# Performance work log

Hardware: AMD Instinct MI355X
Metric: run time of the kernel (lower is better)

The kernel has to match this reference:

```python
import jax, jax.numpy as jnp
import numpy as np

HID = 64        # hid_size
NUM_LAYER = 3
NG = 16         # number of graphs in batch
NPG = 160       # nodes per graph
N = NG * NPG    # 2560 total nodes
DEG = 16
EPG = NPG * DEG # edges per graph
E = NG * EPG    # 40960 total edges
P = NG * NPG * NPG  # 409600 total (i,j) pairs from triu_indices(n, -n)
AV = 64         # atom feature vocab per column (9 columns)
BV = 8          # bond feature vocab per column (3 columns)
EPS = 1e-5


def setup_inputs() -> dict:
    rng = np.random.default_rng(0)
    key = jax.random.key(0)
    ks = jax.random.split(key, 16)

    # categorical node / edge features
    x = jnp.asarray(rng.integers(0, AV, size=(N, 9)), dtype=jnp.int32)
    edge_attr = jnp.asarray(rng.integers(0, BV, size=(E, 3)), dtype=jnp.int32)

    # within-graph random edges (sorted order not required for the math here)
    src_l = rng.integers(0, NPG, size=(NG, EPG))
    dst_l = rng.integers(0, NPG, size=(NG, EPG))
    gid = np.repeat(np.arange(NG), EPG)
    # flat position of edge (u,v) of graph g inside the concatenated all-pairs list
    epos = jnp.asarray(gid * NPG * NPG + src_l.reshape(-1) * NPG + dst_l.reshape(-1),
                       dtype=jnp.int32)

    # idx = concat([triu_indices(n, -n) + ptr[g]]) -> all pairs, row-major per graph
    g = np.arange(NG)[:, None, None]
    i = np.arange(NPG)[None, :, None]
    j = np.arange(NPG)[None, None, :]
    idx0 = jnp.asarray(np.broadcast_to(g * NPG + i, (NG, NPG, NPG)).reshape(-1).astype(np.int32))
    idx1 = jnp.asarray(np.broadcast_to(g * NPG + j, (NG, NPG, NPG)).reshape(-1).astype(np.int32))

    def lin(k, fan_in, fan_out):
        b = 1.0 / np.sqrt(fan_in)
        kw, kb = jax.random.split(k)
        return (jax.random.uniform(kw, (fan_in, fan_out), jnp.float32, -b, b),
                jax.random.uniform(kb, (fan_out,), jnp.float32, -b, b))

    atom_tables = jax.random.normal(ks[0], (9, AV, HID), jnp.float32) * 0.02
    bond_tables = jax.random.normal(ks[1], (3, BV, HID), jnp.float32) * 0.02
    W1, b1 = lin(ks[2], HID, HID)
    W2, b2 = lin(ks[3], HID, HID)
    We, be = lin(ks[4], HID, HID)
    L0_w, L0_b = lin(ks[5], 3 * HID, HID)
    L1_w, L1_b = lin(ks[6], HID, HID)
    L2_w, L2_b = lin(ks[7], HID, 1)
    g0 = jnp.ones((HID,), jnp.float32); beta0 = jnp.zeros((HID,), jnp.float32)
    g1 = jnp.ones((HID,), jnp.float32); beta1 = jnp.zeros((HID,), jnp.float32)

    return dict(atom_tables=atom_tables, bond_tables=bond_tables,
                W1=W1, b1=b1, W2=W2, b2=b2, We=We, be=be,
                L0_w=L0_w, L0_b=L0_b, L1_w=L1_w, L1_b=L1_b, L2_w=L2_w, L2_b=L2_b,
                g0=g0, beta0=beta0, g1=g1, beta1=beta1,
                x=x, edge_attr=edge_attr, idx0=idx0, idx1=idx1, epos=epos)


def _batchnorm(h, gamma, beta):
    mu = jnp.mean(h, axis=0)
    var = jnp.mean(jnp.square(h - mu), axis=0)  # biased var, torch training mode
    return (h - mu) * jax.lax.rsqrt(var + EPS) * gamma + beta


def reference(atom_tables, bond_tables, W1, b1, W2, b2, We, be,
              L0_w, L0_b, L1_w, L1_b, L2_w, L2_b,
              g0, beta0, g1, beta1,
              x, edge_attr, idx0, idx1, epos):
    # AtomEncoder / BondEncoder: sum of per-column embedding lookups
    cols9 = jnp.arange(9)[None, :]
    x_emb = atom_tables[cols9, x].sum(axis=1)          # [N, HID]
    cols3 = jnp.arange(3)[None, :]
    ea_emb = bond_tables[cols3, edge_attr].sum(axis=1)  # [E, HID]

    n1 = (x_emb @ W1 + b1)[idx0]                        # [P, HID]
    n2 = (x_emb @ W2 + b2)[idx1]                        # [P, HID]

    e = ea_emb @ We + be                                # [E, HID]
    # equivalent of SparseTensor.to_dense()[idx0, idx1] without the N^2 dense blowup;
    # duplicate edges sum, missing pairs are zero (matches to_dense semantics)
    e_pairs = jnp.zeros((P, HID), e.dtype).at[epos].add(e)

    emb = jnp.concatenate((n1, n2, e_pairs), axis=-1)   # [P, 3*HID]

    emb = jax.nn.relu(_batchnorm(emb @ L0_w + L0_b, g0, beta0))
    emb = jax.nn.relu(_batchnorm(emb @ L1_w + L1_b, g1, beta1))
    emb = emb @ L2_w + L2_b                             # [P, 1]
    return jnp.squeeze(emb, axis=-1)                    # [P]
```

## Files before the change

### kernel.cpp

```cpp
#include <hip/hip_runtime.h>
#include <hip/hip_bf16.h>

#define HID 64
#define NGr 16
#define NPG 160
#define NN  2560
#define EE  40960
#define PPG 25600
#define PT  409600
#define AV  64
#define BV  8
#define EPSB 1e-5f

typedef __attribute__((ext_vector_type(8))) short short8v;
typedef __attribute__((ext_vector_type(4))) float f32x4;

static __device__ __forceinline__ unsigned short bf16_hi(float v) {
    return (unsigned short)(__float_as_uint(v) >> 16);
}
static __device__ __forceinline__ float bf16_val(unsigned short h) {
    return __uint_as_float(((unsigned int)h) << 16);
}

__global__ void k_prep(const float* __restrict__ W1, const float* __restrict__ b1,
                       const float* __restrict__ W2, const float* __restrict__ b2,
                       const float* __restrict__ We, const float* __restrict__ be,
                       const float* __restrict__ L0w, const float* __restrict__ L0b,
                       const float* __restrict__ L1w,
                       float* __restrict__ W1c, float* __restrict__ W2c, float* __restrict__ Wec,
                       float* __restrict__ b1c, float* __restrict__ b2c, float* __restrict__ bec,
                       float* __restrict__ stats,
                       unsigned short* __restrict__ WBhi, unsigned short* __restrict__ WBlo) {
    int blk = blockIdx.x, tid = threadIdx.x;
    if (blk == 3) {
        stats[tid] = 0.f;
        for (int idx = tid; idx < 4096; idx += 256) {
            float w = L1w[idx];
            unsigned short hi = bf16_hi(w);
            float rem = w - bf16_val(hi);
            WBhi[idx] = hi;
            WBlo[idx] = bf16_hi(rem);
        }
        return;
    }
    const float* Wsrc = (blk == 0) ? W1 : (blk == 1) ? W2 : We;
    const float* bsrc = (blk == 0) ? b1 : (blk == 1) ? b2 : be;
    const float* L    = L0w + blk * 64 * 64;
    float* Wdst = (blk == 0) ? W1c : (blk == 1) ? W2c : Wec;
    float* bdst = (blk == 0) ? b1c : (blk == 1) ? b2c : bec;
    for (int idx = tid; idx < 4096; idx += 256) {
        int k = idx >> 6, h = idx & 63;
        float acc = 0.f;
        for (int m = 0; m < 64; ++m) acc = fmaf(Wsrc[k * 64 + m], L[m * 64 + h], acc);
        Wdst[idx] = acc;
    }
    if (tid < 64) {
        int h = tid;
        float acc = (blk == 0) ? L0b[h] : 0.f;
        for (int m = 0; m < 64; ++m) acc = fmaf(bsrc[m], L[m * 64 + h], acc);
        bdst[h] = acc;
    }
}

__global__ void k_nodes(const float* __restrict__ atab, const int* __restrict__ x,
                        const float* __restrict__ W1c, const float* __restrict__ W2c,
                        const float* __restrict__ b1c, const float* __restrict__ b2c,
                        float* __restrict__ A, float* __restrict__ Bm) {
    int n = blockIdx.x, h = threadIdx.x;
    __shared__ float xe[64];
    float v = 0.f;
#pragma unroll
    for (int c = 0; c < 9; ++c) v += atab[c * AV * HID + x[n * 9 + c] * HID + h];
    xe[h] = v;
    __syncthreads();
    float a = b1c[h], b = b2c[h];
#pragma unroll
    for (int k = 0; k < 64; ++k) {
        float xk = xe[k];
        a = fmaf(xk, W1c[k * 64 + h], a);
        b = fmaf(xk, W2c[k * 64 + h], b);
    }
    A[n * 64 + h] = a;
    Bm[n * 64 + h] = b;
}

__global__ void __launch_bounds__(256) k_dense(const float* __restrict__ A, const float* __restrict__ Bm,
                                               float* __restrict__ zbuf, float* __restrict__ stats) {
    int h = threadIdx.x & 63;
    int wid = threadIdx.x >> 6;
    int wavesTotal = gridDim.x * 4;
    int wave = blockIdx.x * 4 + wid;
    float s = 0.f, ss = 0.f;
    for (int row = wave; row < PT; row += wavesTotal) {
        int g = row / PPG;
        int rem = row - g * PPG;
        int i = rem / NPG;
        int j = rem - i * NPG;
        float v = A[(g * NPG + i) * 64 + h] + Bm[(g * NPG + j) * 64 + h];
        zbuf[(size_t)row * 64 + h] = v;
        s += v;
        ss = fmaf(v, v, ss);
    }
    __shared__ float ls[128];
    if (threadIdx.x < 128) ls[threadIdx.x] = 0.f;
    __syncthreads();
    atomicAdd(&ls[h], s);
    atomicAdd(&ls[64 + h], ss);
    __syncthreads();
    if (threadIdx.x < 128) atomicAdd(&stats[threadIdx.x], ls[threadIdx.x]);
}

__global__ void __launch_bounds__(256) k_edges(const float* __restrict__ btab, const int* __restrict__ eattr,
                                               const int* __restrict__ epos,
                                               const float* __restrict__ Wec, const float* __restrict__ bec,
                                               float* __restrict__ zbuf, float* __restrict__ stats) {
    int h = threadIdx.x & 63;
    int el = threadIdx.x >> 6;
    __shared__ float ea[4][64];
    float s = 0.f, ss = 0.f;
    for (int base = blockIdx.x * 4; base < EE; base += gridDim.x * 4) {
        int e = base + el;
        float v = 0.f;
#pragma unroll
        for (int c = 0; c < 3; ++c) v += btab[c * BV * HID + eattr[e * 3 + c] * HID + h];
        ea[el][h] = v;
        __syncthreads();
        float ew = bec[h];
#pragma unroll
        for (int k = 0; k < 64; ++k) ew = fmaf(ea[el][k], Wec[k * 64 + h], ew);
        int p = epos[e];
        float old = atomicAdd(&zbuf[(size_t)p * 64 + h], ew);
        s += ew;
        ss += 2.f * old * ew + ew * ew;
        __syncthreads();
    }
    __shared__ float ls[128];
    if (threadIdx.x < 128) ls[threadIdx.x] = 0.f;
    __syncthreads();
    atomicAdd(&ls[h], s);
    atomicAdd(&ls[64 + h], ss);
    __syncthreads();
    if (threadIdx.x < 128) atomicAdd(&stats[threadIdx.x], ls[threadIdx.x]);
}

__global__ void __launch_bounds__(256) k_mid(const unsigned short* __restrict__ WBhi,
                                             const unsigned short* __restrict__ WBlo,
                                             const float* __restrict__ L1b,
                                             const float* __restrict__ g0, const float* __restrict__ beta0,
                                             float* __restrict__ zbuf, float* __restrict__ stats) {
    int lane = threadIdx.x & 63;
    int wid  = blockIdx.x * 4 + (threadIdx.x >> 6);
    int nWaves = gridDim.x * 4;
    int r16 = lane & 15;
    int kg  = lane >> 4;

    const float invP = 1.f / (float)PT;
    float s0a[8], t0a[8], s0b[8], t0b[8];
#pragma unroll
    for (int j = 0; j < 8; ++j) {
        int k = kg * 8 + j;
        float mu = stats[k] * invP;
        float var = stats[64 + k] * invP - mu * mu;
        float inv = rsqrtf(var + EPSB);
        s0a[j] = g0[k] * inv;
        t0a[j] = fmaf(-mu, s0a[j], beta0[k]);
        int k2 = k + 32;
        float mu2 = stats[k2] * invP;
        float var2 = stats[64 + k2] * invP - mu2 * mu2;
        float inv2 = rsqrtf(var2 + EPSB);
        s0b[j] = g0[k2] * inv2;
        t0b[j] = fmaf(-mu2, s0b[j], beta0[k2]);
    }
    short8v Bhi[4][2], Blo[4][2];
#pragma unroll
    for (int ct = 0; ct < 4; ++ct)
#pragma unroll
        for (int ks = 0; ks < 2; ++ks)
#pragma unroll
            for (int j = 0; j < 8; ++j) {
                int k = ks * 32 + kg * 8 + j;
                int idx = k * 64 + ct * 16 + r16;
                Bhi[ct][ks][j] = (short)WBhi[idx];
                Blo[ct][ks][j] = (short)WBlo[idx];
            }
    float biasv[4];
#pragma unroll
    for (int ct = 0; ct < 4; ++ct) biasv[ct] = L1b[ct * 16 + r16];

    float sum[4] = {0.f, 0.f, 0.f, 0.f}, ssum[4] = {0.f, 0.f, 0.f, 0.f};

    for (int tile = wid; tile < PT / 16; tile += nWaves) {
        float* tb = zbuf + (size_t)tile * 16 * 64;
        const float4 za0 = *reinterpret_cast<const float4*>(tb + r16 * 64 + kg * 8);
        const float4 za1 = *reinterpret_cast<const float4*>(tb + r16 * 64 + kg * 8 + 4);
        const float4 zb0 = *reinterpret_cast<const float4*>(tb + r16 * 64 + 32 + kg * 8);
        const float4 zb1 = *reinterpret_cast<const float4*>(tb + r16 * 64 + 32 + kg * 8 + 4);
        float ha[8] = {za0.x, za0.y, za0.z, za0.w, za1.x, za1.y, za1.z, za1.w};
        float hb[8] = {zb0.x, zb0.y, zb0.z, zb0.w, zb1.x, zb1.y, zb1.z, zb1.w};
        short8v aHi0, aLo0, aHi1, aLo1;
#pragma unroll
        for (int j = 0; j < 8; ++j) {
            float hv = fmaxf(fmaf(ha[j], s0a[j], t0a[j]), 0.f);
            unsigned short hi = bf16_hi(hv);
            float rem = hv - bf16_val(hi);
            aHi0[j] = (short)hi;
            aLo0[j] = (short)bf16_hi(rem);
            float hv2 = fmaxf(fmaf(hb[j], s0b[j], t0b[j]), 0.f);
            unsigned short hi2 = bf16_hi(hv2);
            float rem2 = hv2 - bf16_val(hi2);
            aHi1[j] = (short)hi2;
            aLo1[j] = (short)bf16_hi(rem2);
        }
        f32x4 acc[4];
#pragma unroll
        for (int ct = 0; ct < 4; ++ct) acc[ct] = (f32x4){0.f, 0.f, 0.f, 0.f};
#pragma unroll
        for (int ct = 0; ct < 4; ++ct) {
            acc[ct] = __builtin_amdgcn_mfma_f32_16x16x32_bf16(aHi0, Bhi[ct][0], acc[ct], 0, 0, 0);
            acc[ct] = __builtin_amdgcn_mfma_f32_16x16x32_bf16(aHi0, Blo[ct][0], acc[ct], 0, 0, 0);
            acc[ct] = __builtin_amdgcn_mfma_f32_16x16x32_bf16(aLo0, Bhi[ct][0], acc[ct], 0, 0, 0);
            acc[ct] = __builtin_amdgcn_mfma_f32_16x16x32_bf16(aHi1, Bhi[ct][1], acc[ct], 0, 0, 0);
            acc[ct] = __builtin_amdgcn_mfma_f32_16x16x32_bf16(aHi1, Blo[ct][1], acc[ct], 0, 0, 0);
            acc[ct] = __builtin_amdgcn_mfma_f32_16x16x32_bf16(aLo1, Bhi[ct][1], acc[ct], 0, 0, 0);
        }
#pragma unroll
        for (int ct = 0; ct < 4; ++ct) {
#pragma unroll
            for (int reg = 0; reg < 4; ++reg) {
                float z = acc[ct][reg] + biasv[ct];
                tb[(kg * 4 + reg) * 64 + ct * 16 + r16] = z;
                sum[ct] += z;
                ssum[ct] = fmaf(z, z, ssum[ct]);
            }
        }
    }
#pragma unroll
    for (int ct = 0; ct < 4; ++ct) {
        float s = sum[ct];
        s += __shfl_xor(s, 16);
        s += __shfl_xor(s, 32);
        float q = ssum[ct];
        q += __shfl_xor(q, 16);
        q += __shfl_xor(q, 32);
        if (kg == 0) {
            atomicAdd(&stats[128 + ct * 16 + r16], s);
            atomicAdd(&stats[192 + ct * 16 + r16], q);
        }
    }
}

__global__ void __launch_bounds__(256) k_final(const float* __restrict__ g1, const float* __restrict__ beta1,
                                               const float* __restrict__ L2w, const float* __restrict__ L2b,
                                               const float* __restrict__ zbuf, float* __restrict__ out,
                                               const float* __restrict__ stats) {
    int lane = threadIdx.x & 63;
    int wid = threadIdx.x >> 6;
    int q = lane & 15;
    int rl = lane >> 4;
    const float invP = 1.f / (float)PT;
    float s1[4], t1[4], wv[4];
#pragma unroll
    for (int c = 0; c < 4; ++c) {
        int col = q * 4 + c;
        float mu = stats[128 + col] * invP;
        float var = stats[192 + col] * invP - mu * mu;
        float inv = rsqrtf(var + EPSB);
        s1[c] = g1[col] * inv;
        t1[c] = fmaf(-mu, s1[c], beta1[col]);
        wv[c] = L2w[col];
    }
    float bias = L2b[0];
    int waveId = blockIdx.x * 4 + wid;
    int stride = gridDim.x * 16;
    for (int base = waveId * 4; base < PT; base += stride) {
        const float4 zv = *reinterpret_cast<const float4*>(zbuf + (size_t)base * 64 + lane * 4);
        float p;
        p  = fmaxf(fmaf(zv.x, s1[0], t1[0]), 0.f) * wv[0];
        p  = fmaf(fmaxf(fmaf(zv.y, s1[1], t1[1]), 0.f), wv[1], p);
        p  = fmaf(fmaxf(fmaf(zv.z, s1[2], t1[2]), 0.f), wv[2], p);
        p  = fmaf(fmaxf(fmaf(zv.w, s1[3], t1[3]), 0.f), wv[3], p);
        p += __shfl_xor(p, 1);
        p += __shfl_xor(p, 2);
        p += __shfl_xor(p, 4);
        p += __shfl_xor(p, 8);
        if (q == 0) out[base + rl] = p + bias;
    }
}

extern "C" void kernel_launch(void* const* d_in, const int* in_sizes, int n_in,
                              void* d_out, int out_size, void* d_ws, size_t ws_size,
                              hipStream_t stream) {
    const float* atab  = (const float*)d_in[0];
    const float* btab  = (const float*)d_in[1];
    const float* W1    = (const float*)d_in[2];
    const float* b1    = (const float*)d_in[3];
    const float* W2    = (const float*)d_in[4];
    const float* b2    = (const float*)d_in[5];
    const float* We    = (const float*)d_in[6];
    const float* be    = (const float*)d_in[7];
    const float* L0w   = (const float*)d_in[8];
    const float* L0b   = (const float*)d_in[9];
    const float* L1w   = (const float*)d_in[10];
    const float* L1b   = (const float*)d_in[11];
    const float* L2w   = (const float*)d_in[12];
    const float* L2b   = (const float*)d_in[13];
    const float* g0    = (const float*)d_in[14];
    const float* beta0 = (const float*)d_in[15];
    const float* g1    = (const float*)d_in[16];
    const float* beta1 = (const float*)d_in[17];
    const int*   x     = (const int*)d_in[18];
    const int*   eattr = (const int*)d_in[19];
    const int*   epos  = (const int*)d_in[22];
    float* out = (float*)d_out;

    float* ws = (float*)d_ws;
    float* zbuf = ws;
    float* A    = zbuf + (size_t)PT * 64;
    float* Bm   = A + NN * 64;
    float* W1c  = Bm + NN * 64;
    float* W2c  = W1c + 4096;
    float* Wec  = W2c + 4096;
    float* b1c  = Wec + 4096;
    float* b2c  = b1c + 64;
    float* bec  = b2c + 64;
    float* stats = bec + 64;
    unsigned short* WBhi = (unsigned short*)(stats + 256);
    unsigned short* WBlo = WBhi + 4096;

    k_prep<<<4, 256, 0, stream>>>(W1, b1, W2, b2, We, be, L0w, L0b, L1w,
                                  W1c, W2c, Wec, b1c, b2c, bec, stats, WBhi, WBlo);
    k_nodes<<<NN, 64, 0, stream>>>(atab, x, W1c, W2c, b1c, b2c, A, Bm);
    k_dense<<<2048, 256, 0, stream>>>(A, Bm, zbuf, stats);
    k_edges<<<512, 256, 0, stream>>>(btab, eattr, epos, Wec, bec, zbuf, stats);
    k_mid<<<512, 256, 0, stream>>>(WBhi, WBlo, L1b, g0, beta0, zbuf, stats);
    k_final<<<1024, 256, 0, stream>>>(g1, beta1, L2w, L2b, zbuf, out, stats);
}
```

Before: 231.4 us.

## Eliminate dense pair buffer; recompute layer-0/1 per tile from node and edge lists

```diff
diff --git a/kernel.cpp b/kernel.cpp
--- a/kernel.cpp
+++ b/kernel.cpp
@@ -8,6 +8,8 @@
 #define EE  40960
 #define PPG 25600
 #define PT  409600
+#define TT  25600
+#define TPG 1600
 #define AV  64
 #define BV  8
 #define EPSB 1e-5f
@@ -29,11 +31,9 @@
                        const float* __restrict__ L1w,
                        float* __restrict__ W1c, float* __restrict__ W2c, float* __restrict__ Wec,
                        float* __restrict__ b1c, float* __restrict__ b2c, float* __restrict__ bec,
-                       float* __restrict__ stats,
                        unsigned short* __restrict__ WBhi, unsigned short* __restrict__ WBlo) {
     int blk = blockIdx.x, tid = threadIdx.x;
     if (blk == 3) {
-        stats[tid] = 0.f;
         for (int idx = tid; idx < 4096; idx += 256) {
             float w = L1w[idx];
             unsigned short hi = bf16_hi(w);
@@ -84,78 +84,195 @@
     Bm[n * 64 + h] = b;
 }
 
-__global__ void __launch_bounds__(256) k_dense(const float* __restrict__ A, const float* __restrict__ Bm,
-                                               float* __restrict__ zbuf, float* __restrict__ stats) {
-    int h = threadIdx.x & 63;
-    int wid = threadIdx.x >> 6;
-    int wavesTotal = gridDim.x * 4;
-    int wave = blockIdx.x * 4 + wid;
-    float s = 0.f, ss = 0.f;
-    for (int row = wave; row < PT; row += wavesTotal) {
-        int g = row / PPG;
-        int rem = row - g * PPG;
-        int i = rem / NPG;
-        int j = rem - i * NPG;
-        float v = A[(g * NPG + i) * 64 + h] + Bm[(g * NPG + j) * 64 + h];
-        zbuf[(size_t)row * 64 + h] = v;
-        s += v;
-        ss = fmaf(v, v, ss);
-    }
-    __shared__ float ls[128];
-    if (threadIdx.x < 128) ls[threadIdx.x] = 0.f;
+__global__ void k_gstats(const float* __restrict__ A, const float* __restrict__ Bm,
+                         float* __restrict__ stats) {
+    int g = blockIdx.x;
+    int h = threadIdx.x & 63, w = threadIdx.x >> 6;
+    float sA = 0.f, sA2 = 0.f, sB = 0.f, sB2 = 0.f;
+    for (int n = w; n < NPG; n += 4) {
+        float a = A[(size_t)(g * NPG + n) * 64 + h];
+        float b = Bm[(size_t)(g * NPG + n) * 64 + h];
+        sA += a; sA2 = fmaf(a, a, sA2);
+        sB += b; sB2 = fmaf(b, b, sB2);
+    }
+    __shared__ float ls[4][4][64];
+    ls[w][0][h] = sA; ls[w][1][h] = sA2; ls[w][2][h] = sB; ls[w][3][h] = sB2;
     __syncthreads();
-    atomicAdd(&ls[h], s);
-    atomicAdd(&ls[64 + h], ss);
-    __syncthreads();
-    if (threadIdx.x < 128) atomicAdd(&stats[threadIdx.x], ls[threadIdx.x]);
+    if (w == 0) {
+        sA  = ls[0][0][h] + ls[1][0][h] + ls[2][0][h] + ls[3][0][h];
+        sA2 = ls[0][1][h] + ls[1][1][h] + ls[2][1][h] + ls[3][1][h];
+        sB  = ls[0][2][h] + ls[1][2][h] + ls[2][2][h] + ls[3][2][h];
+        sB2 = ls[0][3][h] + ls[1][3][h] + ls[2][3][h] + ls[3][3][h];
+        atomicAdd(&stats[h], 160.f * (sA + sB));
+        atomicAdd(&stats[64 + h], 160.f * (sA2 + sB2) + 2.f * sA * sB);
+    }
 }
 
 __global__ void __launch_bounds__(256) k_edges(const float* __restrict__ btab, const int* __restrict__ eattr,
                                                const int* __restrict__ epos,
                                                const float* __restrict__ Wec, const float* __restrict__ bec,
-                                               float* __restrict__ zbuf, float* __restrict__ stats) {
+                                               float* __restrict__ ewf, float* __restrict__ stats,
+                                               int* __restrict__ bcount) {
     int h = threadIdx.x & 63;
     int el = threadIdx.x >> 6;
     __shared__ float ea[4][64];
-    float s = 0.f, ss = 0.f;
+    float ssum = 0.f;
     for (int base = blockIdx.x * 4; base < EE; base += gridDim.x * 4) {
         int e = base + el;
         float v = 0.f;
 #pragma unroll
         for (int c = 0; c < 3; ++c) v += btab[c * BV * HID + eattr[e * 3 + c] * HID + h];
         ea[el][h] = v;
+        float ew = bec[h];
+#pragma unroll
+        for (int k = 0; k < 64; ++k) ew = fmaf(ea[el][k], Wec[k * 64 + h], ew);
+        ewf[(size_t)e * 64 + h] = ew;
+        ssum += ew;
+        if (h == 0) atomicAdd(&bcount[epos[e] >> 4], 1);
+    }
+    atomicAdd(&stats[h], ssum);
+}
+
+__global__ void k_scan(const int* __restrict__ bcount, int* __restrict__ boffs,
+                       int* __restrict__ bcursor) {
+    __shared__ int part[256];
+    int tid = threadIdx.x;
+    int base = tid * (TT / 256);
+    int s = 0;
+    for (int q = 0; q < TT / 256; ++q) s += bcount[base + q];
+    part[tid] = s;
+    __syncthreads();
+    for (int d = 1; d < 256; d <<= 1) {
+        int v = (tid >= d) ? part[tid - d] : 0;
         __syncthreads();
-        float ew = bec[h];
-#pragma unroll
-        for (int k = 0; k < 64; ++k) ew = fmaf(ea[el][k], Wec[k * 64 + h], ew);
-        int p = epos[e];
-        float old = atomicAdd(&zbuf[(size_t)p * 64 + h], ew);
-        s += ew;
-        ss += 2.f * old * ew + ew * ew;
+        part[tid] += v;
         __syncthreads();
     }
-    __shared__ float ls[128];
-    if (threadIdx.x < 128) ls[threadIdx.x] = 0.f;
-    __syncthreads();
-    atomicAdd(&ls[h], s);
-    atomicAdd(&ls[64 + h], ss);
-    __syncthreads();
-    if (threadIdx.x < 128) atomicAdd(&stats[threadIdx.x], ls[threadIdx.x]);
-}
-
-__global__ void __launch_bounds__(256) k_mid(const unsigned short* __restrict__ WBhi,
-                                             const unsigned short* __restrict__ WBlo,
-                                             const float* __restrict__ L1b,
-                                             const float* __restrict__ g0, const float* __restrict__ beta0,
-                                             float* __restrict__ zbuf, float* __restrict__ stats) {
-    int lane = threadIdx.x & 63;
-    int wid  = blockIdx.x * 4 + (threadIdx.x >> 6);
-    int nWaves = gridDim.x * 4;
-    int r16 = lane & 15;
-    int kg  = lane >> 4;
-
+    int run = part[tid] - s;
+    for (int q = 0; q < TT / 256; ++q) {
+        int c = bcount[base + q];
+        boffs[base + q] = run;
+        bcursor[base + q] = run;
+        run += c;
+    }
+    if (tid == 255) boffs[TT] = run;
+}
+
+__global__ void k_fill(const int* __restrict__ epos, int* __restrict__ bcursor,
+                       int* __restrict__ elist) {
+    int e = blockIdx.x * 256 + threadIdx.x;
+    if (e >= EE) return;
+    int p = epos[e];
+    int t = p >> 4, jj = p & 15;
+    int slot = atomicAdd(&bcursor[t], 1);
+    elist[slot] = (e << 4) | jj;
+}
+
+__global__ void __launch_bounds__(256) k_scorr(const float* __restrict__ A, const float* __restrict__ Bm,
+                                               const float* __restrict__ ewf,
+                                               const int* __restrict__ boffs, const int* __restrict__ elist,
+                                               float* __restrict__ stats) {
+    __shared__ float run[4][16][64];
+    int h = threadIdx.x & 63, w = threadIdx.x >> 6;
+#pragma unroll
+    for (int jj = 0; jj < 16; ++jj) run[w][jj][h] = 0.f;
+    float ssacc = 0.f;
+    int wave = blockIdx.x * 4 + w;
+    int nw = gridDim.x * 4;
+    for (int t = wave; t < TT; t += nw) {
+        int be = boffs[t], en = boffs[t + 1];
+        if (be == en) continue;
+        int g = t / TPG;
+        int rem = t - g * TPG;
+        int i = rem / 10;
+        int j0 = (rem - i * 10) << 4;
+        float a = A[(size_t)(g * NPG + i) * 64 + h];
+        for (int q = be; q < en; ++q) {
+            int pk = elist[q];
+            int e = pk >> 4, jj = pk & 15;
+            float ew = ewf[(size_t)e * 64 + h];
+            float base = a + Bm[(size_t)(g * NPG + j0 + jj) * 64 + h];
+            float r = run[w][jj][h];
+            ssacc += 2.f * (base + r) * ew + ew * ew;
+            run[w][jj][h] = r + ew;
+        }
+        for (int q = be; q < en; ++q) run[w][elist[q] & 15][h] = 0.f;
+    }
+    atomicAdd(&stats[64 + h], ssacc);
+}
+
+static __device__ __forceinline__ void compute_tile(
+    int tile, int r16, int kg,
+    const float* __restrict__ A, const float* __restrict__ Bm, const float* __restrict__ ewf,
+    const int* __restrict__ boffs, const int* __restrict__ elist,
+    const float* s0a, const float* t0a, const float* s0b, const float* t0b,
+    const short8v Bhi[4][2], const short8v Blo[4][2],
+    f32x4 acc[4]) {
+    int g = tile / TPG;
+    int rem = tile - g * TPG;
+    int i = rem / 10;
+    int j0 = (rem - i * 10) << 4;
+    const float* Arow = A + (size_t)(g * NPG + i) * 64;
+    const float* Brow = Bm + (size_t)(g * NPG + j0 + r16) * 64;
+    float4 a0 = *reinterpret_cast<const float4*>(Arow + kg * 8);
+    float4 a1 = *reinterpret_cast<const float4*>(Arow + kg * 8 + 4);
+    float4 a2 = *reinterpret_cast<const float4*>(Arow + 32 + kg * 8);
+    float4 a3 = *reinterpret_cast<const float4*>(Arow + 32 + kg * 8 + 4);
+    float4 b0 = *reinterpret_cast<const float4*>(Brow + kg * 8);
+    float4 b1 = *reinterpret_cast<const float4*>(Brow + kg * 8 + 4);
+    float4 b2 = *reinterpret_cast<const float4*>(Brow + 32 + kg * 8);
+    float4 b3 = *reinterpret_cast<const float4*>(Brow + 32 + kg * 8 + 4);
+    float za[8] = {a0.x + b0.x, a0.y + b0.y, a0.z + b0.z, a0.w + b0.w,
+                   a1.x + b1.x, a1.y + b1.y, a1.z + b1.z, a1.w + b1.w};
+    float zb[8] = {a2.x + b2.x, a2.y + b2.y, a2.z + b2.z, a2.w + b2.w,
+                   a3.x + b3.x, a3.y + b3.y, a3.z + b3.z, a3.w + b3.w};
+    int be = boffs[tile], en = boffs[tile + 1];
+    for (int q = be; q < en; ++q) {
+        int pk = elist[q];
+        int e = pk >> 4, jj = pk & 15;
+        const float* er = ewf + (size_t)e * 64;
+        float4 e0 = *reinterpret_cast<const float4*>(er + kg * 8);
+        float4 e1 = *reinterpret_cast<const float4*>(er + kg * 8 + 4);
+        float4 e2 = *reinterpret_cast<const float4*>(er + 32 + kg * 8);
+        float4 e3 = *reinterpret_cast<const float4*>(er + 32 + kg * 8 + 4);
+        if (r16 == jj) {
+            za[0] += e0.x; za[1] += e0.y; za[2] += e0.z; za[3] += e0.w;
+            za[4] += e1.x; za[5] += e1.y; za[6] += e1.z; za[7] += e1.w;
+            zb[0] += e2.x; zb[1] += e2.y; zb[2] += e2.z; zb[3] += e2.w;
+            zb[4] += e3.x; zb[5] += e3.y; zb[6] += e3.z; zb[7] += e3.w;
+        }
+    }
+    short8v aHi0, aLo0, aHi1, aLo1;
+#pragma unroll
+    for (int j = 0; j < 8; ++j) {
+        float hv = fmaxf(fmaf(za[j], s0a[j], t0a[j]), 0.f);
+        unsigned short hi = bf16_hi(hv);
+        float remv = hv - bf16_val(hi);
+        aHi0[j] = (short)hi;
+        aLo0[j] = (short)bf16_hi(remv);
+        float hv2 = fmaxf(fmaf(zb[j], s0b[j], t0b[j]), 0.f);
+        unsigned short hi2 = bf16_hi(hv2);
+        float rem2 = hv2 - bf16_val(hi2);
+        aHi1[j] = (short)hi2;
+        aLo1[j] = (short)bf16_hi(rem2);
+    }
+#pragma unroll
+    for (int ct = 0; ct < 4; ++ct) acc[ct] = (f32x4){0.f, 0.f, 0.f, 0.f};
+#pragma unroll
+    for (int ct = 0; ct < 4; ++ct) {
+        acc[ct] = __builtin_amdgcn_mfma_f32_16x16x32_bf16(aHi0, Bhi[ct][0], acc[ct], 0, 0, 0);
+        acc[ct] = __builtin_amdgcn_mfma_f32_16x16x32_bf16(aHi0, Blo[ct][0], acc[ct], 0, 0, 0);
+        acc[ct] = __builtin_amdgcn_mfma_f32_16x16x32_bf16(aLo0, Bhi[ct][0], acc[ct], 0, 0, 0);
+        acc[ct] = __builtin_amdgcn_mfma_f32_16x16x32_bf16(aHi1, Bhi[ct][1], acc[ct], 0, 0, 0);
+        acc[ct] = __builtin_amdgcn_mfma_f32_16x16x32_bf16(aHi1, Blo[ct][1], acc[ct], 0, 0, 0);
+        acc[ct] = __builtin_amdgcn_mfma_f32_16x16x32_bf16(aLo1, Bhi[ct][1], acc[ct], 0, 0, 0);
+    }
+}
+
+static __device__ __forceinline__ void load_bn0(const float* __restrict__ stats,
+                                                const float* __restrict__ g0, const float* __restrict__ beta0,
+                                                int kg, float* s0a, float* t0a, float* s0b, float* t0b) {
     const float invP = 1.f / (float)PT;
-    float s0a[8], t0a[8], s0b[8], t0b[8];
 #pragma unroll
     for (int j = 0; j < 8; ++j) {
         int k = kg * 8 + j;
@@ -171,7 +288,11 @@
         s0b[j] = g0[k2] * inv2;
         t0b[j] = fmaf(-mu2, s0b[j], beta0[k2]);
     }
-    short8v Bhi[4][2], Blo[4][2];
+}
+
+static __device__ __forceinline__ void load_wb(const unsigned short* __restrict__ WBhi,
+                                               const unsigned short* __restrict__ WBlo,
+                                               int r16, int kg, short8v Bhi[4][2], short8v Blo[4][2]) {
 #pragma unroll
     for (int ct = 0; ct < 4; ++ct)
 #pragma unroll
@@ -183,52 +304,36 @@
                 Bhi[ct][ks][j] = (short)WBhi[idx];
                 Blo[ct][ks][j] = (short)WBlo[idx];
             }
+}
+
+__global__ void __launch_bounds__(256) k_pass1(const unsigned short* __restrict__ WBhi,
+                                               const unsigned short* __restrict__ WBlo,
+                                               const float* __restrict__ L1b,
+                                               const float* __restrict__ g0, const float* __restrict__ beta0,
+                                               const float* __restrict__ A, const float* __restrict__ Bm,
+                                               const float* __restrict__ ewf,
+                                               const int* __restrict__ boffs, const int* __restrict__ elist,
+                                               float* __restrict__ stats) {
+    int lane = threadIdx.x & 63;
+    int wid = blockIdx.x * 4 + (threadIdx.x >> 6);
+    int nWaves = gridDim.x * 4;
+    int r16 = lane & 15, kg = lane >> 4;
+    float s0a[8], t0a[8], s0b[8], t0b[8];
+    load_bn0(stats, g0, beta0, kg, s0a, t0a, s0b, t0b);
+    short8v Bhi[4][2], Blo[4][2];
+    load_wb(WBhi, WBlo, r16, kg, Bhi, Blo);
     float biasv[4];
 #pragma unroll
     for (int ct = 0; ct < 4; ++ct) biasv[ct] = L1b[ct * 16 + r16];
-
     float sum[4] = {0.f, 0.f, 0.f, 0.f}, ssum[4] = {0.f, 0.f, 0.f, 0.f};
-
-    for (int tile = wid; tile < PT / 16; tile += nWaves) {
-        float* tb = zbuf + (size_t)tile * 16 * 64;
-        const float4 za0 = *reinterpret_cast<const float4*>(tb + r16 * 64 + kg * 8);
-        const float4 za1 = *reinterpret_cast<const float4*>(tb + r16 * 64 + kg * 8 + 4);
-        const float4 zb0 = *reinterpret_cast<const float4*>(tb + r16 * 64 + 32 + kg * 8);
-        const float4 zb1 = *reinterpret_cast<const float4*>(tb + r16 * 64 + 32 + kg * 8 + 4);
-        float ha[8] = {za0.x, za0.y, za0.z, za0.w, za1.x, za1.y, za1.z, za1.w};
-        float hb[8] = {zb0.x, zb0.y, zb0.z, zb0.w, zb1.x, zb1.y, zb1.z, zb1.w};
-        short8v aHi0, aLo0, aHi1, aLo1;
-#pragma unroll
-        for (int j = 0; j < 8; ++j) {
-            float hv = fmaxf(fmaf(ha[j], s0a[j], t0a[j]), 0.f);
-            unsigned short hi = bf16_hi(hv);
-            float rem = hv - bf16_val(hi);
-            aHi0[j] = (short)hi;
-            aLo0[j] = (short)bf16_hi(rem);
-            float hv2 = fmaxf(fmaf(hb[j], s0b[j], t0b[j]), 0.f);
-            unsigned short hi2 = bf16_hi(hv2);
-            float rem2 = hv2 - bf16_val(hi2);
-            aHi1[j] = (short)hi2;
-            aLo1[j] = (short)bf16_hi(rem2);
-        }
+    for (int tile = wid; tile < TT; tile += nWaves) {
         f32x4 acc[4];
-#pragma unroll
-        for (int ct = 0; ct < 4; ++ct) acc[ct] = (f32x4){0.f, 0.f, 0.f, 0.f};
-#pragma unroll
-        for (int ct = 0; ct < 4; ++ct) {
-            acc[ct] = __builtin_amdgcn_mfma_f32_16x16x32_bf16(aHi0, Bhi[ct][0], acc[ct], 0, 0, 0);
-            acc[ct] = __builtin_amdgcn_mfma_f32_16x16x32_bf16(aHi0, Blo[ct][0], acc[ct], 0, 0, 0);
-            acc[ct] = __builtin_amdgcn_mfma_f32_16x16x32_bf16(aLo0, Bhi[ct][0], acc[ct], 0, 0, 0);
-            acc[ct] = __builtin_amdgcn_mfma_f32_16x16x32_bf16(aHi1, Bhi[ct][1], acc[ct], 0, 0, 0);
-            acc[ct] = __builtin_amdgcn_mfma_f32_16x16x32_bf16(aHi1, Blo[ct][1], acc[ct], 0, 0, 0);
-            acc[ct] = __builtin_amdgcn_mfma_f32_16x16x32_bf16(aLo1, Bhi[ct][1], acc[ct], 0, 0, 0);
-        }
+        compute_tile(tile, r16, kg, A, Bm, ewf, boffs, elist, s0a, t0a, s0b, t0b, Bhi, Blo, acc);
 #pragma unroll
         for (int ct = 0; ct < 4; ++ct) {
 #pragma unroll
             for (int reg = 0; reg < 4; ++reg) {
                 float z = acc[ct][reg] + biasv[ct];
-                tb[(kg * 4 + reg) * 64 + ct * 16 + r16] = z;
                 sum[ct] += z;
                 ssum[ct] = fmaf(z, z, ssum[ct]);
             }
@@ -249,41 +354,55 @@
     }
 }
 
-__global__ void __launch_bounds__(256) k_final(const float* __restrict__ g1, const float* __restrict__ beta1,
+__global__ void __launch_bounds__(256) k_pass2(const unsigned short* __restrict__ WBhi,
+                                               const unsigned short* __restrict__ WBlo,
+                                               const float* __restrict__ L1b,
+                                               const float* __restrict__ g0, const float* __restrict__ beta0,
+                                               const float* __restrict__ g1, const float* __restrict__ beta1,
                                                const float* __restrict__ L2w, const float* __restrict__ L2b,
-                                               const float* __restrict__ zbuf, float* __restrict__ out,
-                                               const float* __restrict__ stats) {
+                                               const float* __restrict__ A, const float* __restrict__ Bm,
+                                               const float* __restrict__ ewf,
+                                               const int* __restrict__ boffs, const int* __restrict__ elist,
+                                               const float* __restrict__ stats, float* __restrict__ out) {
     int lane = threadIdx.x & 63;
-    int wid = threadIdx.x >> 6;
-    int q = lane & 15;
-    int rl = lane >> 4;
+    int wid = blockIdx.x * 4 + (threadIdx.x >> 6);
+    int nWaves = gridDim.x * 4;
+    int r16 = lane & 15, kg = lane >> 4;
+    float s0a[8], t0a[8], s0b[8], t0b[8];
+    load_bn0(stats, g0, beta0, kg, s0a, t0a, s0b, t0b);
+    short8v Bhi[4][2], Blo[4][2];
+    load_wb(WBhi, WBlo, r16, kg, Bhi, Blo);
+    float biasv[4], s1c[4], t1c[4], wv[4];
     const float invP = 1.f / (float)PT;
-    float s1[4], t1[4], wv[4];
-#pragma unroll
-    for (int c = 0; c < 4; ++c) {
-        int col = q * 4 + c;
+#pragma unroll
+    for (int ct = 0; ct < 4; ++ct) {
+        int col = ct * 16 + r16;
+        biasv[ct] = L1b[col];
         float mu = stats[128 + col] * invP;
         float var = stats[192 + col] * invP - mu * mu;
         float inv = rsqrtf(var + EPSB);
-        s1[c] = g1[col] * inv;
-        t1[c] = fmaf(-mu, s1[c], beta1[col]);
-        wv[c] = L2w[col];
-    }
-    float bias = L2b[0];
-    int waveId = blockIdx.x * 4 + wid;
-    int stride = gridDim.x * 16;
-    for (int base = waveId * 4; base < PT; base += stride) {
-        const float4 zv = *reinterpret_cast<const float4*>(zbuf + (size_t)base * 64 + lane * 4);
-        float p;
-        p  = fmaxf(fmaf(zv.x, s1[0], t1[0]), 0.f) * wv[0];
-        p  = fmaf(fmaxf(fmaf(zv.y, s1[1], t1[1]), 0.f), wv[1], p);
-        p  = fmaf(fmaxf(fmaf(zv.z, s1[2], t1[2]), 0.f), wv[2], p);
-        p  = fmaf(fmaxf(fmaf(zv.w, s1[3], t1[3]), 0.f), wv[3], p);
-        p += __shfl_xor(p, 1);
-        p += __shfl_xor(p, 2);
-        p += __shfl_xor(p, 4);
-        p += __shfl_xor(p, 8);
-        if (q == 0) out[base + rl] = p + bias;
+        s1c[ct] = g1[col] * inv;
+        t1c[ct] = fmaf(-mu, s1c[ct], beta1[col]);
+        wv[ct] = L2w[col];
+    }
+    float obias = L2b[0];
+    for (int tile = wid; tile < TT; tile += nWaves) {
+        f32x4 acc[4];
+        compute_tile(tile, r16, kg, A, Bm, ewf, boffs, elist, s0a, t0a, s0b, t0b, Bhi, Blo, acc);
+#pragma unroll
+        for (int reg = 0; reg < 4; ++reg) {
+            float p = 0.f;
+#pragma unroll
+            for (int ct = 0; ct < 4; ++ct) {
+                float z = acc[ct][reg] + biasv[ct];
+                p = fmaf(fmaxf(fmaf(z, s1c[ct], t1c[ct]), 0.f), wv[ct], p);
+            }
+            p += __shfl_xor(p, 1);
+            p += __shfl_xor(p, 2);
+            p += __shfl_xor(p, 4);
+            p += __shfl_xor(p, 8);
+            if (r16 == 0) out[tile * 16 + kg * 4 + reg] = p + obias;
+        }
     }
 }
 
@@ -313,11 +432,11 @@
     const int*   epos  = (const int*)d_in[22];
     float* out = (float*)d_out;
 
-    float* ws = (float*)d_ws;
-    float* zbuf = ws;
-    float* A    = zbuf + (size_t)PT * 64;
-    float* Bm   = A + NN * 64;
-    float* W1c  = Bm + NN * 64;
+    float* ws   = (float*)d_ws;
+    float* A    = ws;
+    float* Bm   = A + (size_t)NN * 64;
+    float* ewf  = Bm + (size_t)NN * 64;
+    float* W1c  = ewf + (size_t)EE * 64;
     float* W2c  = W1c + 4096;
     float* Wec  = W2c + 4096;
     float* b1c  = Wec + 4096;
@@ -326,12 +445,23 @@
     float* stats = bec + 64;
     unsigned short* WBhi = (unsigned short*)(stats + 256);
     unsigned short* WBlo = WBhi + 4096;
+    int* bcount  = (int*)(WBlo + 4096);
+    int* boffs   = bcount + TT;
+    int* bcursor = boffs + TT + 1;
+    int* elist   = bcursor + TT;
+
+    hipMemsetAsync(stats, 0, 256 * sizeof(float), stream);
+    hipMemsetAsync(bcount, 0, TT * sizeof(int), stream);
 
     k_prep<<<4, 256, 0, stream>>>(W1, b1, W2, b2, We, be, L0w, L0b, L1w,
-                                  W1c, W2c, Wec, b1c, b2c, bec, stats, WBhi, WBlo);
+                                  W1c, W2c, Wec, b1c, b2c, bec, WBhi, WBlo);
     k_nodes<<<NN, 64, 0, stream>>>(atab, x, W1c, W2c, b1c, b2c, A, Bm);
-    k_dense<<<2048, 256, 0, stream>>>(A, Bm, zbuf, stats);
-    k_edges<<<512, 256, 0, stream>>>(btab, eattr, epos, Wec, bec, zbuf, stats);
-    k_mid<<<512, 256, 0, stream>>>(WBhi, WBlo, L1b, g0, beta0, zbuf, stats);
-    k_final<<<1024, 256, 0, stream>>>(g1, beta1, L2w, L2b, zbuf, out, stats);
-}
+    k_gstats<<<NGr, 256, 0, stream>>>(A, Bm, stats);
+    k_edges<<<512, 256, 0, stream>>>(btab, eattr, epos, Wec, bec, ewf, stats, bcount);
+    k_scan<<<1, 256, 0, stream>>>(bcount, boffs, bcursor);
+    k_fill<<<EE / 256, 256, 0, stream>>>(epos, bcursor, elist);
+    k_scorr<<<256, 256, 0, stream>>>(A, Bm, ewf, boffs, elist, stats);
+    k_pass1<<<1600, 256, 0, stream>>>(WBhi, WBlo, L1b, g0, beta0, A, Bm, ewf, boffs, elist, stats);
+    k_pass2<<<1600, 256, 0, stream>>>(WBhi, WBlo, L1b, g0, beta0, g1, beta1, L2w, L2b,
+                                      A, Bm, ewf, boffs, elist, stats, out);
+}
```

Result: slower. 413.0 us (+78.5%).
